# Optimization experiments

Hardware: AMD Instinct MI355X
Metric: run time of the kernel (lower is better)

The kernel has to match this reference:

```python
import jax, jax.numpy as jnp
import numpy as np

EMBED_DIM = 1024
NUM_HEADS = 16
HEAD_DIM = EMBED_DIM // NUM_HEADS
SEQ = 2048
BSZ = 2


def setup_inputs() -> dict:
    key = jax.random.key(0)
    ks = jax.random.split(key, 12)
    f = jnp.float32
    query = jax.random.normal(ks[0], (SEQ, BSZ, EMBED_DIM), f)
    k_in = jax.random.normal(ks[1], (SEQ, BSZ, EMBED_DIM), f)
    v_in = jax.random.normal(ks[2], (SEQ, BSZ, EMBED_DIM), f)
    s = 0.02  # weight init scale
    q_w = jax.random.normal(ks[3], (EMBED_DIM, EMBED_DIM), f) * s
    q_b = jax.random.normal(ks[4], (EMBED_DIM,), f) * s
    k_w = jax.random.normal(ks[5], (EMBED_DIM, EMBED_DIM), f) * s
    k_b = jax.random.normal(ks[6], (EMBED_DIM,), f) * s
    v_w = jax.random.normal(ks[7], (EMBED_DIM, EMBED_DIM), f) * s
    v_b = jax.random.normal(ks[8], (EMBED_DIM,), f) * s
    o_w_mean = jax.random.normal(ks[9], (EMBED_DIM, EMBED_DIM), f) * s
    # lgstd ~ uniform(2*log(stdv), log(stdv)) with stdv = 1/sqrt(out+1)
    stdv = 1.0 / np.sqrt(EMBED_DIM + 1)
    o_w_lgstd = jax.random.uniform(ks[10], (EMBED_DIM, EMBED_DIM), f,
                                   2.0 * np.log(stdv), np.log(stdv))
    eps = jax.random.normal(ks[11], (EMBED_DIM, EMBED_DIM), f) * 1.5  # N(0, 1.5)
    return dict(query=query, key=k_in, value=v_in,
                q_w=q_w, q_b=q_b, k_w=k_w, k_b=k_b, v_w=v_w, v_b=v_b,
                o_w_mean=o_w_mean, o_w_lgstd=o_w_lgstd, eps=eps)


def reference(query, key, value, q_w, q_b, k_w, k_b, v_w, v_b,
              o_w_mean, o_w_lgstd, eps):
    tgt_len, bsz, embed_dim = query.shape
    scaling = HEAD_DIM ** -0.5
    # projections (F.linear: x @ W.T + b)
    q = (query @ q_w.T + q_b) * scaling          # [S,B,E]
    k = key @ k_w.T + k_b                        # [S,B,E]
    v = value @ v_w.T + v_b                      # [S,B,E]
    # [S,B,E] -> [B*H, S, hd]
    def split_heads(x, L):
        return x.reshape(L, bsz * NUM_HEADS, HEAD_DIM).transpose(1, 0, 2)
    q = split_heads(q, tgt_len)
    k = split_heads(k, key.shape[0])
    v = split_heads(v, value.shape[0])
    src_len = k.shape[1]
    scores = jnp.einsum('bqd,bkd->bqk', q, k)    # [B*H, S, S] (explicit O(n^2))
    attn = jax.nn.softmax(scores, axis=-1)
    ctx = jnp.einsum('bqk,bkd->bqd', attn, v)    # [B*H, S, hd]
    ctx = ctx.transpose(1, 0, 2).reshape(tgt_len, bsz, embed_dim)
    # Bayesian output projection: sampled weight (training mode), no bias
    o_w = o_w_mean + eps * jnp.exp(o_w_lgstd)
    out = ctx @ o_w.T                            # [S,B,E]
    avg_attn = attn.reshape(bsz, NUM_HEADS, tgt_len, src_len).sum(axis=1) / NUM_HEADS
    return out, avg_attn
```

## Files before the change

kernel.cpp:

```cpp
#include <hip/hip_runtime.h>

#define SQ 2048
#define BB 2
#define EE 1024
#define HH 16
#define DD 64
#define MM (SQ*BB)
#define NSLICE 4
#define KSLICE (SQ/NSLICE)
#define KT_IN (KSLICE/128)
#define LOG2E 1.44269504f

typedef _Float16 f16;
typedef _Float16 half8 __attribute__((ext_vector_type(8)));
typedef _Float16 half4 __attribute__((ext_vector_type(4)));
typedef float f32x4 __attribute__((ext_vector_type(4)));

static __device__ __forceinline__ f32x4 mfma16(half8 a, half8 b, f32x4 c) {
    return __builtin_amdgcn_mfma_f32_16x16x32_f16(a, b, c, 0, 0, 0);
}

static __device__ __forceinline__ void gload16(const f16* g, f16* l) {
    __builtin_amdgcn_global_load_lds(
        (const __attribute__((address_space(1))) unsigned int*)g,
        (__attribute__((address_space(3))) unsigned int*)l, 16, 0, 0);
}

__global__ void k_elem(const float* __restrict__ q_w, const float* __restrict__ k_w,
                       const float* __restrict__ v_w, const float* __restrict__ query,
                       const float* __restrict__ key, const float* __restrict__ value,
                       const float* __restrict__ owm, const float* __restrict__ owl,
                       const float* __restrict__ eps,
                       f16* qw16, f16* kw16, f16* vw16,
                       f16* xq16, f16* xk16, f16* xv16, f16* ow16)
{
    int y = blockIdx.y;
    size_t i = ((size_t)blockIdx.x * 256 + threadIdx.x) * 4;
    if (y < 3) {
        if (i >= (size_t)EE*EE) return;
        const float* s = (y==0) ? q_w : (y==1) ? k_w : v_w;
        f16* d = (y==0) ? qw16 : (y==1) ? kw16 : vw16;
        float4 v = *(const float4*)&s[i];
        half4 o = {(f16)v.x, (f16)v.y, (f16)v.z, (f16)v.w};
        *(half4*)&d[i] = o;
    } else if (y < 6) {
        const float* s = (y==3) ? query : (y==4) ? key : value;
        f16* d = (y==3) ? xq16 : (y==4) ? xk16 : xv16;
        float4 v = *(const float4*)&s[i];
        half4 o = {(f16)v.x, (f16)v.y, (f16)v.z, (f16)v.w};
        *(half4*)&d[i] = o;
    } else {
        if (i >= (size_t)EE*EE) return;
        float4 m = *(const float4*)&owm[i];
        float4 l = *(const float4*)&owl[i];
        float4 e = *(const float4*)&eps[i];
        half4 o = {(f16)(m.x + e.x * __expf(l.x)), (f16)(m.y + e.y * __expf(l.y)),
                   (f16)(m.z + e.z * __expf(l.z)), (f16)(m.w + e.w * __expf(l.w))};
        *(half4*)&ow16[i] = o;
    }
}

__device__ __forceinline__ void gemm_body(
    const f16* __restrict__ A, const f16* __restrict__ W,
    const float* __restrict__ bias, float scale, void* __restrict__ out, int mode)
{
    __shared__ f16 As[128*32];
    __shared__ f16 Bs[64*32];
    int t = threadIdx.x, lane = t & 63, w = t >> 6;
    int quad = lane >> 4, m16 = lane & 15;
    int wm = w >> 1, wn = w & 1;
    int gm0 = blockIdx.x * 128, gn0 = blockIdx.y * 64;
    int arow = lane >> 2, apch = lane & 3;
    f32x4 acc[4][2] = {};
    for (int kt = 0; kt < EE; kt += 32) {
        #pragma unroll
        for (int j = 0; j < 2; ++j) {
            int row = w*32 + j*16 + arow;
            int lch = apch ^ (row & 3);
            gload16(&A[(size_t)(gm0+row)*EE + kt + lch*8], &As[row*32 + apch*8]);
        }
        {
            int row = w*16 + arow;
            int lch = apch ^ (row & 3);
            gload16(&W[(size_t)(gn0+row)*EE + kt + lch*8], &Bs[row*32 + apch*8]);
        }
        __syncthreads();
        int cs = (quad ^ (m16 & 3)) * 8;
        half8 af[4], bf[2];
        #pragma unroll
        for (int i = 0; i < 4; ++i) af[i] = *(half8*)&As[(wm*64 + i*16 + m16)*32 + cs];
        #pragma unroll
        for (int j = 0; j < 2; ++j) bf[j] = *(half8*)&Bs[(wn*32 + j*16 + m16)*32 + cs];
        #pragma unroll
        for (int i = 0; i < 4; ++i)
            #pragma unroll
            for (int j = 0; j < 2; ++j)
                acc[i][j] = mfma16(af[i], bf[j], acc[i][j]);
        __syncthreads();
    }
    #pragma unroll
    for (int j = 0; j < 2; ++j) {
        int col = gn0 + wn*32 + j*16 + m16;
        int h = col >> 6, d = col & 63;
        float bb = bias ? bias[col] : 0.0f;
        #pragma unroll
        for (int i = 0; i < 4; ++i) {
            int r0 = gm0 + wm*64 + i*16 + quad*4;
            #pragma unroll
            for (int r = 0; r < 4; ++r) {
                float v = (acc[i][j][r] + bb) * scale;
                int m = r0 + r;
                int s = m >> 1, b = m & 1;
                if (mode == 2)
                    ((float*)out)[(size_t)m*EE + col] = v;
                else if (mode == 1)
                    ((f16*)out)[((((size_t)b*HH + h)*(SQ/32) + (s >> 5))*DD + d)*32 + (s & 31)] = (f16)v;
                else
                    ((f16*)out)[(((size_t)b*HH + h)*SQ + s)*DD + d] = (f16)v;
            }
        }
    }
}

__global__ __launch_bounds__(256) void k_gemm_qkv(
    const f16* xq, const f16* qw, const float* qb,
    const f16* xk, const f16* kw, const float* kb,
    const f16* xv, const f16* vw, const float* vb,
    f16* Q16, f16* K16, f16* Vt16)
{
    int z = blockIdx.z;
    const f16* A = (z==0) ? xq : (z==1) ? xk : xv;
    const f16* W = (z==0) ? qw : (z==1) ? kw : vw;
    const float* bi = (z==0) ? qb : (z==1) ? kb : vb;
    float sc = (z==0) ? 0.125f * LOG2E : 1.0f;
    void* o = (z==0) ? (void*)Q16 : (z==1) ? (void*)K16 : (void*)Vt16;
    gemm_body(A, W, bi, sc, o, (z==2) ? 1 : 0);
}

__global__ __launch_bounds__(256) void k_gemm_o(const f16* A, const f16* W, float* out)
{
    gemm_body(A, W, nullptr, 1.0f, out, 2);
}

__global__ __launch_bounds__(256, 4) void k_attn_l(
    const f16* __restrict__ Q16, const f16* __restrict__ K16, float* __restrict__ lse2)
{
    __shared__ float red[4][64];
    const int t = threadIdx.x, lane = t & 63, w = t >> 6;
    const int quad = lane >> 4, m16 = lane & 15;
    const int bid = blockIdx.x;
    const int xcd = bid & 7, r = bid >> 3;
    const int c = ((r & 3) << 3) + xcd;
    const int q0 = (r >> 2) * 64;
    const int h = c >> 1, b = c & 1;
    const f16* Qh = Q16 + ((size_t)b*HH + h)*SQ*DD;
    const f16* Kh = K16 + ((size_t)b*HH + h)*SQ*DD;

    half8 bq[4][2];
    #pragma unroll
    for (int nt = 0; nt < 4; ++nt)
        #pragma unroll
        for (int dk = 0; dk < 2; ++dk)
            bq[nt][dk] = *(const half8*)&Qh[(q0 + nt*16 + m16)*DD + dk*32 + quad*8];

    float lsum[4] = {};
    for (int kt = 0; kt < 16; ++kt) {
        half8 ak[2][2];
        #pragma unroll
        for (int mt = 0; mt < 2; ++mt)
            #pragma unroll
            for (int dk = 0; dk < 2; ++dk)
                ak[mt][dk] = *(const half8*)&Kh[(kt*128 + w*32 + mt*16 + m16)*DD + dk*32 + quad*8];
        #pragma unroll
        for (int mt = 0; mt < 2; ++mt)
            #pragma unroll
            for (int nt = 0; nt < 4; ++nt) {
                f32x4 s = {};
                s = mfma16(ak[mt][0], bq[nt][0], s);
                s = mfma16(ak[mt][1], bq[nt][1], s);
                lsum[nt] += __builtin_amdgcn_exp2f(s[0]) + __builtin_amdgcn_exp2f(s[1])
                          + __builtin_amdgcn_exp2f(s[2]) + __builtin_amdgcn_exp2f(s[3]);
            }
    }
    #pragma unroll
    for (int nt = 0; nt < 4; ++nt) {
        float v = lsum[nt];
        v += __shfl_xor(v, 16, 64);
        v += __shfl_xor(v, 32, 64);
        lsum[nt] = v;
    }
    if (quad == 0)
        #pragma unroll
        for (int nt = 0; nt < 4; ++nt) red[w][nt*16 + m16] = lsum[nt];
    __syncthreads();
    if (t < 64) {
        float v = red[0][t] + red[1][t] + red[2][t] + red[3][t];
        lse2[((size_t)b*HH + h)*SQ + q0 + t] = __log2f(v);
    }
}

__global__ __launch_bounds__(256, 2) void k_attn_main(
    const f16* __restrict__ Q16, const f16* __restrict__ K16, const f16* __restrict__ Vt16,
    const float* __restrict__ lse2, float* __restrict__ ctxp, float* __restrict__ avg_out)
{
    __shared__ f16 ps[2][32][136];
    __shared__ float csh[HH][32];
    const int t = threadIdx.x, lane = t & 63, w = t >> 6;
    const int quad = lane >> 4, m16 = lane & 15;
    const int bid = blockIdx.x;
    const int g = bid & 7;
    const int q0 = (bid >> 3) * 32;
    const int sl = g >> 1, b = g & 1;
    const int ks0 = sl * KSLICE;

    for (int i = t; i < HH*32; i += 256) {
        int hh = i >> 5, qq = i & 31;
        csh[hh][qq] = lse2[((size_t)b*HH + hh)*SQ + q0 + qq];
    }
    __syncthreads();

    float avg_r[KT_IN][16] = {};

    for (int hp = 0; hp < 8; ++hp) {
        f32x4 acc[2][2] = {};
        for (int hh2 = 0; hh2 < 2; ++hh2) {
            const int h = hp*2 + hh2;
            const f16* Qh = Q16 + ((size_t)b*HH + h)*SQ*DD;
            const f16* Kh = K16 + ((size_t)b*HH + h)*SQ*DD;
            const f16* Vh = Vt16 + ((size_t)b*HH + h)*(SQ/32)*DD*32;
            half8 bq[2][2];
            #pragma unroll
            for (int nt = 0; nt < 2; ++nt)
                #pragma unroll
                for (int dk = 0; dk < 2; ++dk)
                    bq[nt][dk] = *(const half8*)&Qh[(q0 + nt*16 + m16)*DD + dk*32 + quad*8];
            const float c01[2] = { csh[h][m16], csh[h][16 + m16] };

            half8 ak[2][2][2], bv[2][4];
            #pragma unroll
            for (int mt = 0; mt < 2; ++mt)
                #pragma unroll
                for (int dk = 0; dk < 2; ++dk)
                    ak[0][mt][dk] = *(const half8*)&Kh[(ks0 + w*32 + mt*16 + m16)*DD + dk*32 + quad*8];
            #pragma unroll
            for (int ks = 0; ks < 4; ++ks)
                bv[0][ks] = *(const half8*)&Vh[(((ks0 + ks*32) >> 5)*DD + w*16 + m16)*32 + quad*8];

            #pragma unroll
            for (int kt = 0; kt < KT_IN; ++kt) {
                const int cur = kt & 1, nxt = cur ^ 1;
                if (kt + 1 < KT_IN) {
                    #pragma unroll
                    for (int mt = 0; mt < 2; ++mt)
                        #pragma unroll
                        for (int dk = 0; dk < 2; ++dk)
                            ak[nxt][mt][dk] = *(const half8*)&Kh[(ks0 + (kt+1)*128 + w*32 + mt*16 + m16)*DD + dk*32 + quad*8];
                    #pragma unroll
                    for (int ks = 0; ks < 4; ++ks)
                        bv[nxt][ks] = *(const half8*)&Vh[(((ks0 + (kt+1)*128 + ks*32) >> 5)*DD + w*16 + m16)*32 + quad*8];
                }
                #pragma unroll
                for (int mt = 0; mt < 2; ++mt)
                    #pragma unroll
                    for (int nt = 0; nt < 2; ++nt) {
                        f32x4 s = {};
                        s = mfma16(ak[cur][mt][0], bq[nt][0], s);
                        s = mfma16(ak[cur][mt][1], bq[nt][1], s);
                        half4 ph;
                        #pragma unroll
                        for (int r = 0; r < 4; ++r) {
                            float p = __builtin_amdgcn_exp2f(s[r] - c01[nt]);
                            avg_r[kt][mt*8 + nt*4 + r] += p;
                            ph[r] = (f16)p;
                        }
                        *(half4*)&ps[cur][nt*16 + m16][w*32 + mt*16 + quad*4] = ph;
                    }
                __builtin_amdgcn_sched_barrier(0);
                __builtin_amdgcn_s_waitcnt(0xC07F);
                __builtin_amdgcn_s_barrier();
                __builtin_amdgcn_sched_barrier(0);
                #pragma unroll
                for (int qt = 0; qt < 2; ++qt) {
                    f32x4 c4 = acc[hh2][qt];
                    #pragma unroll
                    for (int ks = 0; ks < 4; ++ks) {
                        half8 ap = *(half8*)&ps[cur][qt*16 + m16][ks*32 + quad*8];
                        c4 = mfma16(ap, bv[cur][ks], c4);
                    }
                    acc[hh2][qt] = c4;
                }
            }
        }
        #pragma unroll
        for (int hh2 = 0; hh2 < 2; ++hh2)
            #pragma unroll
            for (int qt = 0; qt < 2; ++qt)
                #pragma unroll
                for (int r = 0; r < 4; ++r) {
                    int q = q0 + qt*16 + quad*4 + r;
                    ctxp[(size_t)sl*MM*EE + ((size_t)q*BB + b)*EE + (hp*2 + hh2)*DD + w*16 + m16] = acc[hh2][qt][r];
                }
    }
    #pragma unroll
    for (int kt = 0; kt < KT_IN; ++kt)
        #pragma unroll
        for (int mt = 0; mt < 2; ++mt)
            #pragma unroll
            for (int nt = 0; nt < 2; ++nt) {
                int q = q0 + nt*16 + m16;
                int k = ks0 + kt*128 + w*32 + mt*16 + quad*4;
                float4 v = { avg_r[kt][mt*8+nt*4+0]*(1.0f/HH), avg_r[kt][mt*8+nt*4+1]*(1.0f/HH),
                             avg_r[kt][mt*8+nt*4+2]*(1.0f/HH), avg_r[kt][mt*8+nt*4+3]*(1.0f/HH) };
                *(float4*)&avg_out[((size_t)b*SQ + q)*SQ + k] = v;
            }
}

__global__ void k_ctx_red(const float* __restrict__ ctxp, f16* __restrict__ ctx16) {
    size_t i = ((size_t)blockIdx.x * 256 + threadIdx.x) * 4;
    float4 s = *(const float4*)&ctxp[i];
    #pragma unroll
    for (int sl = 1; sl < NSLICE; ++sl) {
        float4 v = *(const float4*)&ctxp[(size_t)sl*MM*EE + i];
        s.x += v.x; s.y += v.y; s.z += v.z; s.w += v.w;
    }
    half4 o = {(f16)s.x, (f16)s.y, (f16)s.z, (f16)s.w};
    *(half4*)&ctx16[i] = o;
}

extern "C" void kernel_launch(void* const* d_in, const int* in_sizes, int n_in,
                              void* d_out, int out_size, void* d_ws, size_t ws_size,
                              hipStream_t stream) {
    const float* query    = (const float*)d_in[0];
    const float* key      = (const float*)d_in[1];
    const float* value    = (const float*)d_in[2];
    const float* q_w      = (const float*)d_in[3];
    const float* q_b      = (const float*)d_in[4];
    const float* k_w      = (const float*)d_in[5];
    const float* k_b      = (const float*)d_in[6];
    const float* v_w      = (const float*)d_in[7];
    const float* v_b      = (const float*)d_in[8];
    const float* o_w_mean = (const float*)d_in[9];
    const float* o_w_lgstd= (const float*)d_in[10];
    const float* eps      = (const float*)d_in[11];
    float* out = (float*)d_out;
    float* avg = out + (size_t)MM * EE;

    const size_t EWN = (size_t)EE*EE;
    const size_t XWN = (size_t)MM*EE;
    f16* qw16  = (f16*)d_ws;
    f16* kw16  = qw16 + EWN;
    f16* vw16  = kw16 + EWN;
    f16* ow16  = vw16 + EWN;
    f16* Q16   = ow16 + EWN;
    f16* K16   = Q16  + XWN;
    f16* Vt16  = K16  + XWN;
    f16* ctx16 = Vt16 + XWN;
    float* lse2 = (float*)(ctx16 + XWN);
    f16* xq16  = (f16*)(lse2 + (size_t)BB*HH*SQ);
    f16* xk16  = xq16 + XWN;
    f16* xv16  = xk16 + XWN;
    float* ctxp = (float*)xq16;

    k_elem<<<dim3(XWN/1024, 7), 256, 0, stream>>>(q_w, k_w, v_w, query, key, value,
        o_w_mean, o_w_lgstd, eps, qw16, kw16, vw16, xq16, xk16, xv16, ow16);

    k_gemm_qkv<<<dim3(MM/128, EE/64, 3), 256, 0, stream>>>(
        xq16, qw16, q_b, xk16, kw16, k_b, xv16, vw16, v_b, Q16, K16, Vt16);

    k_attn_l   <<<dim3(SQ/64 * HH * BB), 256, 0, stream>>>(Q16, K16, lse2);
    k_attn_main<<<dim3(SQ/32 * NSLICE * BB), 256, 0, stream>>>(Q16, K16, Vt16, lse2, ctxp, avg);
    k_ctx_red  <<<XWN/1024, 256, 0, stream>>>(ctxp, ctx16);

    k_gemm_o<<<dim3(MM/128, EE/64), 256, 0, stream>>>(ctx16, ow16, out);
}
```

Measured before the change: 369.1 us.

## Keep P in registers for PV MFMA and reduce across waves via LDS

The attention main kernel no longer round-trips the probability tile through shared memory. Each wave multiplies its own P fragments directly against V with 16x16x16 MFMAs over its key subrange, producing partial context for all 64 head dims. The partials are then reduced across the four waves through an LDS buffer. This removes the per-tile barrier and the P store/load, but adds a per-head cross-wave reduction with two barriers, more accumulator registers, and smaller V loads.

```diff
diff --git a/kernel.cpp b/kernel.cpp
--- a/kernel.cpp
+++ b/kernel.cpp
@@ -18,6 +18,9 @@
 
 static __device__ __forceinline__ f32x4 mfma16(half8 a, half8 b, f32x4 c) {
     return __builtin_amdgcn_mfma_f32_16x16x32_f16(a, b, c, 0, 0, 0);
+}
+static __device__ __forceinline__ f32x4 mfma16k16(half4 a, half4 b, f32x4 c) {
+    return __builtin_amdgcn_mfma_f32_16x16x16f16(a, b, c, 0, 0, 0);
 }
 
 static __device__ __forceinline__ void gload16(const f16* g, f16* l) {
@@ -203,7 +206,7 @@
     const f16* __restrict__ Q16, const f16* __restrict__ K16, const f16* __restrict__ Vt16,
     const float* __restrict__ lse2, float* __restrict__ ctxp, float* __restrict__ avg_out)
 {
-    __shared__ f16 ps[2][32][136];
+    __shared__ float red[4][3][16][36];
     __shared__ float csh[HH][32];
     const int t = threadIdx.x, lane = t & 63, w = t >> 6;
     const int quad = lane >> 4, m16 = lane & 15;
@@ -221,86 +224,100 @@
 
     float avg_r[KT_IN][16] = {};
 
-    for (int hp = 0; hp < 8; ++hp) {
-        f32x4 acc[2][2] = {};
-        for (int hh2 = 0; hh2 < 2; ++hh2) {
-            const int h = hp*2 + hh2;
-            const f16* Qh = Q16 + ((size_t)b*HH + h)*SQ*DD;
-            const f16* Kh = K16 + ((size_t)b*HH + h)*SQ*DD;
-            const f16* Vh = Vt16 + ((size_t)b*HH + h)*(SQ/32)*DD*32;
-            half8 bq[2][2];
-            #pragma unroll
-            for (int nt = 0; nt < 2; ++nt)
-                #pragma unroll
-                for (int dk = 0; dk < 2; ++dk)
-                    bq[nt][dk] = *(const half8*)&Qh[(q0 + nt*16 + m16)*DD + dk*32 + quad*8];
-            const float c01[2] = { csh[h][m16], csh[h][16 + m16] };
-
-            half8 ak[2][2][2], bv[2][4];
+    for (int h = 0; h < HH; ++h) {
+        const f16* Qh = Q16 + ((size_t)b*HH + h)*SQ*DD;
+        const f16* Kh = K16 + ((size_t)b*HH + h)*SQ*DD;
+        const f16* Vh = Vt16 + ((size_t)b*HH + h)*(SQ/32)*DD*32;
+        half8 bq[2][2];
+        #pragma unroll
+        for (int nt = 0; nt < 2; ++nt)
+            #pragma unroll
+            for (int dk = 0; dk < 2; ++dk)
+                bq[nt][dk] = *(const half8*)&Qh[(q0 + nt*16 + m16)*DD + dk*32 + quad*8];
+        const float c01[2] = { csh[h][m16], csh[h][16 + m16] };
+
+        f32x4 acc[2][4] = {};
+
+        half8 ak[2][2][2];
+        #pragma unroll
+        for (int mt = 0; mt < 2; ++mt)
+            #pragma unroll
+            for (int dk = 0; dk < 2; ++dk)
+                ak[0][mt][dk] = *(const half8*)&Kh[(ks0 + w*32 + mt*16 + m16)*DD + dk*32 + quad*8];
+
+        #pragma unroll
+        for (int kt = 0; kt < KT_IN; ++kt) {
+            const int cur = kt & 1, nxt = cur ^ 1;
+            const int ktile32 = (ks0 + kt*128 + w*32) >> 5;
+
+            half4 bv[2][4];
             #pragma unroll
             for (int mt = 0; mt < 2; ++mt)
                 #pragma unroll
-                for (int dk = 0; dk < 2; ++dk)
-                    ak[0][mt][dk] = *(const half8*)&Kh[(ks0 + w*32 + mt*16 + m16)*DD + dk*32 + quad*8];
-            #pragma unroll
-            for (int ks = 0; ks < 4; ++ks)
-                bv[0][ks] = *(const half8*)&Vh[(((ks0 + ks*32) >> 5)*DD + w*16 + m16)*32 + quad*8];
-
-            #pragma unroll
-            for (int kt = 0; kt < KT_IN; ++kt) {
-                const int cur = kt & 1, nxt = cur ^ 1;
-                if (kt + 1 < KT_IN) {
-                    #pragma unroll
-                    for (int mt = 0; mt < 2; ++mt)
-                        #pragma unroll
-                        for (int dk = 0; dk < 2; ++dk)
-                            ak[nxt][mt][dk] = *(const half8*)&Kh[(ks0 + (kt+1)*128 + w*32 + mt*16 + m16)*DD + dk*32 + quad*8];
-                    #pragma unroll
-                    for (int ks = 0; ks < 4; ++ks)
-                        bv[nxt][ks] = *(const half8*)&Vh[(((ks0 + (kt+1)*128 + ks*32) >> 5)*DD + w*16 + m16)*32 + quad*8];
-                }
+                for (int db = 0; db < 4; ++db)
+                    bv[mt][db] = *(const half4*)&Vh[((size_t)ktile32*DD + db*16 + m16)*32 + mt*16 + quad*4];
+
+            if (kt + 1 < KT_IN) {
                 #pragma unroll
                 for (int mt = 0; mt < 2; ++mt)
                     #pragma unroll
-                    for (int nt = 0; nt < 2; ++nt) {
-                        f32x4 s = {};
-                        s = mfma16(ak[cur][mt][0], bq[nt][0], s);
-                        s = mfma16(ak[cur][mt][1], bq[nt][1], s);
-                        half4 ph;
-                        #pragma unroll
-                        for (int r = 0; r < 4; ++r) {
-                            float p = __builtin_amdgcn_exp2f(s[r] - c01[nt]);
-                            avg_r[kt][mt*8 + nt*4 + r] += p;
-                            ph[r] = (f16)p;
-                        }
-                        *(half4*)&ps[cur][nt*16 + m16][w*32 + mt*16 + quad*4] = ph;
+                    for (int dk = 0; dk < 2; ++dk)
+                        ak[nxt][mt][dk] = *(const half8*)&Kh[(ks0 + (kt+1)*128 + w*32 + mt*16 + m16)*DD + dk*32 + quad*8];
+            }
+
+            half4 pa[2][2];
+            #pragma unroll
+            for (int mt = 0; mt < 2; ++mt)
+                #pragma unroll
+                for (int nt = 0; nt < 2; ++nt) {
+                    f32x4 s = {};
+                    s = mfma16(ak[cur][mt][0], bq[nt][0], s);
+                    s = mfma16(ak[cur][mt][1], bq[nt][1], s);
+                    half4 ph;
+                    #pragma unroll
+                    for (int r = 0; r < 4; ++r) {
+                        float p = __builtin_amdgcn_exp2f(s[r] - c01[nt]);
+                        avg_r[kt][mt*8 + nt*4 + r] += p;
+                        ph[r] = (f16)p;
                     }
-                __builtin_amdgcn_sched_barrier(0);
-                __builtin_amdgcn_s_waitcnt(0xC07F);
-                __builtin_amdgcn_s_barrier();
-                __builtin_amdgcn_sched_barrier(0);
-                #pragma unroll
-                for (int qt = 0; qt < 2; ++qt) {
-                    f32x4 c4 = acc[hh2][qt];
-                    #pragma unroll
-                    for (int ks = 0; ks < 4; ++ks) {
-                        half8 ap = *(half8*)&ps[cur][qt*16 + m16][ks*32 + quad*8];
-                        c4 = mfma16(ap, bv[cur][ks], c4);
-                    }
-                    acc[hh2][qt] = c4;
+                    pa[mt][nt] = ph;
                 }
-            }
-        }
-        #pragma unroll
-        for (int hh2 = 0; hh2 < 2; ++hh2)
-            #pragma unroll
-            for (int qt = 0; qt < 2; ++qt)
-                #pragma unroll
-                for (int r = 0; r < 4; ++r) {
-                    int q = q0 + qt*16 + quad*4 + r;
-                    ctxp[(size_t)sl*MM*EE + ((size_t)q*BB + b)*EE + (hp*2 + hh2)*DD + w*16 + m16] = acc[hh2][qt][r];
+
+            #pragma unroll
+            for (int nt = 0; nt < 2; ++nt)
+                #pragma unroll
+                for (int db = 0; db < 4; ++db) {
+                    f32x4 c4 = acc[nt][db];
+                    c4 = mfma16k16(pa[0][nt], bv[0][db], c4);
+                    c4 = mfma16k16(pa[1][nt], bv[1][db], c4);
+                    acc[nt][db] = c4;
                 }
-    }
+        }
+
+        #pragma unroll
+        for (int db = 0; db < 4; ++db)
+            if (db != w) {
+                int slot = w - (w > db);
+                #pragma unroll
+                for (int qt = 0; qt < 2; ++qt)
+                    *(f32x4*)&red[db][slot][m16][qt*16 + quad*4] = acc[qt][db];
+            }
+        __syncthreads();
+        #pragma unroll
+        for (int qt = 0; qt < 2; ++qt) {
+            f32x4 c = acc[qt][w];
+            #pragma unroll
+            for (int slot = 0; slot < 3; ++slot)
+                c = c + *(const f32x4*)&red[w][slot][m16][qt*16 + quad*4];
+            #pragma unroll
+            for (int r = 0; r < 4; ++r) {
+                int q = q0 + qt*16 + quad*4 + r;
+                ctxp[(size_t)sl*MM*EE + ((size_t)q*BB + b)*EE + h*DD + w*16 + m16] = c[r];
+            }
+        }
+        __syncthreads();
+    }
+
     #pragma unroll
     for (int kt = 0; kt < KT_IN; ++kt)
         #pragma unroll
```

Result: slower. 417.7 us (+13.2%).
